# Optimization experiments

Measured on AMD Instinct MI355X. Metric: run time of the kernel, lower is better.

Reference implementation:

```python
import jax, jax.numpy as jnp
import numpy as np


def setup_inputs() -> dict:
    key = jax.random.key(0)
    k1, k2, k3, k4 = jax.random.split(key, 4)
    B, T, D = 32, 2048, 128
    queries = jax.random.normal(k1, (B, T, D), dtype=jnp.float32)
    keys = jax.random.normal(k2, (B, T, D), dtype=jnp.float32)
    values = jax.random.normal(k3, (B, T, D), dtype=jnp.float32)
    valid_lens = jax.random.randint(k4, (B,), 0, T, dtype=jnp.int32)
    return {"queries": queries, "keys": keys, "values": values, "valid_lens": valid_lens}


def reference(queries, keys, values, valid_lens):
    d = queries.shape[-1]
    scale = d / 0.5  # faithful to source: 2*d, NOT sqrt(d)
    # (B, Tq, Tk) scores
    scores = jnp.einsum('bqd,bkd->bqk', queries, keys) / scale
    T = scores.shape[-1]
    # lengths (B,) -> mask (B, 1, Tk), broadcast over query rows
    mask = jnp.arange(T) < valid_lens[:, None, None]
    neg_inf = jnp.finfo(scores.dtype).min
    logits = jnp.where(mask, scores, neg_inf)
    probs = jax.nn.softmax(logits, axis=-1)
    fully_masked = ~jnp.any(mask, axis=-1, keepdims=True)
    probs = jnp.where(fully_masked, jnp.zeros_like(probs), probs)
    # dropout p=0.0 -> identity
    return jnp.einsum('bqk,bkv->bqv', probs, values)
```

## Files before the change

kernel.cpp:

```cpp
#include <hip/hip_runtime.h>
#include <hip/hip_bf16.h>
#include <stdint.h>

#define B_ 32
#define T_ 2048
#define D_ 128
#define BQ 128
#define BK 64

typedef __attribute__((ext_vector_type(8))) __bf16 bf16x8;
typedef __attribute__((ext_vector_type(16))) float f32x16;

__device__ __forceinline__ float fast_exp2(float x) {
#if __has_builtin(__builtin_amdgcn_exp2f)
    return __builtin_amdgcn_exp2f(x);
#else
    return exp2f(x);
#endif
}

__device__ __forceinline__ f32x16 zero16() {
    f32x16 z;
    #pragma unroll
    for (int i = 0; i < 16; ++i) z[i] = 0.f;
    return z;
}

__device__ __forceinline__ uint32_t pk2(float a, float b) {
    union { __hip_bfloat16 h; unsigned short u; } ua, ub;
    ua.h = __float2bfloat16(a); ub.h = __float2bfloat16(b);
    return (uint32_t)ua.u | ((uint32_t)ub.u << 16);
}

__device__ __forceinline__ void plswap(uint32_t& a, uint32_t& b) {
    asm("v_permlane32_swap_b32 %0, %1" : "+v"(a), "+v"(b));
}

__device__ __forceinline__ void gll16(const __hip_bfloat16* g, __hip_bfloat16* lds) {
    __builtin_amdgcn_global_load_lds(
        (const __attribute__((address_space(1))) uint32_t*)g,
        (__attribute__((address_space(3))) uint32_t*)lds,
        16, 0, 0);
}

__global__ __launch_bounds__(256, 4)
void prep_k(const float* __restrict__ K, const int* __restrict__ vlens,
            __hip_bfloat16* __restrict__ Kb)
{
    const int b = blockIdx.y, k0 = blockIdx.x * 64;
    const int kmax = (vlens[b] + 63) & ~63;
    if (k0 >= kmax) return;
    const float4* src = (const float4*)(K + ((size_t)b * T_ + k0) * D_);
    uint2* dst = (uint2*)(Kb + ((size_t)b * T_ + k0) * D_);
    #pragma unroll
    for (int it = 0; it < 8; ++it) {
        int c = it * 256 + threadIdx.x;
        float4 v = src[c];
        union { __hip_bfloat16 h[4]; uint2 u; } pk;
        pk.h[0] = __float2bfloat16(v.x); pk.h[1] = __float2bfloat16(v.y);
        pk.h[2] = __float2bfloat16(v.z); pk.h[3] = __float2bfloat16(v.w);
        dst[c] = pk.u;
    }
}

__global__ __launch_bounds__(256, 2)
void prep_vt(const float* __restrict__ V, const int* __restrict__ vlens,
             __hip_bfloat16* __restrict__ VTb)
{
    __shared__ float tile[64][132];
    const int b = blockIdx.y, k0 = blockIdx.x * 64;
    const int kmax = (vlens[b] + 63) & ~63;
    if (k0 >= kmax) return;
    const float4* src = (const float4*)(V + ((size_t)b * T_ + k0) * D_);
    #pragma unroll
    for (int it = 0; it < 8; ++it) {
        int c = it * 256 + threadIdx.x;
        int row = c >> 5, c4 = c & 31;
        *(float4*)&tile[row][c4 * 4] = src[c];
    }
    __syncthreads();
    #pragma unroll
    for (int it = 0; it < 8; ++it) {
        int c = it * 256 + threadIdx.x;
        int kc = c & 15, d = c >> 4;
        union { __hip_bfloat16 h[4]; uint2 u; } pk;
        #pragma unroll
        for (int j = 0; j < 4; ++j) {
            int jj = (j + kc) & 3;
            pk.h[jj] = __float2bfloat16(tile[kc * 4 + jj][d]);
        }
        *(uint2*)(VTb + ((size_t)b * D_ + d) * T_ + k0 + kc * 4) = pk.u;
    }
}

__global__ __launch_bounds__(256, 2)
void attn_main(const float* __restrict__ Q, const int* __restrict__ vlens,
               const __hip_bfloat16* __restrict__ Kb,
               const __hip_bfloat16* __restrict__ VTb,
               float* __restrict__ out)
{
    const int tid  = threadIdx.x;
    const int wave = tid >> 6;
    const int lane = tid & 63;
    const int l32  = lane & 31;
    const int hi   = lane >> 5;

    const int b    = blockIdx.y;
    const int q0   = blockIdx.x * BQ;
    const int vlen = vlens[b];
    const int nkb  = (vlen + 63) >> 6;

    __shared__ __hip_bfloat16 sK [2][64][128];
    __shared__ __hip_bfloat16 sVT[2][128][64];

    bf16x8 qf[8];
    {
        const float* qp = Q + ((size_t)b * T_ + q0 + wave * 32 + l32) * D_ + hi * 8;
        #pragma unroll
        for (int ds = 0; ds < 8; ++ds) {
            const float4* p4 = (const float4*)(qp + ds * 16);
            float4 a = p4[0], c = p4[1];
            __hip_bfloat16 h[8] = {
                __float2bfloat16(a.x), __float2bfloat16(a.y),
                __float2bfloat16(a.z), __float2bfloat16(a.w),
                __float2bfloat16(c.x), __float2bfloat16(c.y),
                __float2bfloat16(c.z), __float2bfloat16(c.w) };
            qf[ds] = *(const bf16x8*)h;
        }
    }

    f32x16 o[4];
    #pragma unroll
    for (int dt = 0; dt < 4; ++dt) o[dt] = zero16();
    float lsum = 0.f;

    const float C = 1.4426950408889634f / 256.0f;

    const __hip_bfloat16* kb_base = Kb  + (size_t)b * T_ * D_;
    const __hip_bfloat16* vt_base = VTb + (size_t)b * D_ * T_;

    auto stage = [&](int k0s, int buf) {
        #pragma unroll
        for (int it = 0; it < 4; ++it) {
            const int blk = wave * 4 + it;
            {
                const int row = blk * 4 + (lane >> 4);
                const int s   = (lane & 15) ^ (row & 7);
                gll16(kb_base + (size_t)(k0s + row) * D_ + s * 8,
                      &sK[buf][0][0] + blk * 512);
            }
            {
                const int row = blk * 8 + (lane >> 3);
                const int s   = (lane & 7) ^ (row & 7);
                gll16(vt_base + (size_t)row * T_ + k0s + s * 8,
                      &sVT[buf][0][0] + blk * 512);
            }
        }
    };

    if (nkb > 0) stage(0, 0);
    __syncthreads();

    int cur = 0;
    for (int kb = 0; kb < nkb; ++kb) {
        const int k0 = kb * 64;

        if (kb + 1 < nkb) stage(k0 + 64, cur ^ 1);

        f32x16 s[2];
        s[0] = zero16(); s[1] = zero16();
        __builtin_amdgcn_s_setprio(1);
        #pragma unroll
        for (int ds = 0; ds < 8; ++ds) {
            const int r0 = l32, r1 = 32 + l32;
            bf16x8 kf0 = *(const bf16x8*)&sK[cur][r0][((ds * 2 + hi) ^ (r0 & 7)) * 8];
            bf16x8 kf1 = *(const bf16x8*)&sK[cur][r1][((ds * 2 + hi) ^ (r1 & 7)) * 8];
            s[0] = __builtin_amdgcn_mfma_f32_32x32x16_bf16(kf0, qf[ds], s[0], 0, 0, 0);
            s[1] = __builtin_amdgcn_mfma_f32_32x32x16_bf16(kf1, qf[ds], s[1], 0, 0, 0);
        }
        __builtin_amdgcn_s_setprio(0);

        bf16x8 pf[4];
        #pragma unroll
        for (int nt = 0; nt < 2; ++nt) {
            const int kbase_l = k0 + nt * 32 + 4 * hi;
            float p[16];
            #pragma unroll
            for (int r = 0; r < 16; ++r) {
                int krow = (r & 3) + 8 * (r >> 2);
                float e = fast_exp2(s[nt][r] * C);
                p[r] = (kbase_l + krow < vlen) ? e : 0.f;
            }
            lsum += (((p[0] + p[1]) + (p[2] + p[3])) + ((p[4] + p[5]) + (p[6] + p[7])))
                  + (((p[8] + p[9]) + (p[10] + p[11])) + ((p[12] + p[13]) + (p[14] + p[15])));
            #pragma unroll
            for (int k2 = 0; k2 < 2; ++k2) {
                const int base = k2 * 8;
                uint32_t A0 = pk2(p[base + 0], p[base + 1]);
                uint32_t B0 = pk2(p[base + 4], p[base + 5]);
                uint32_t A1 = pk2(p[base + 2], p[base + 3]);
                uint32_t B1 = pk2(p[base + 6], p[base + 7]);
                plswap(A0, B0);
                plswap(A1, B1);
                union { uint32_t u[4]; bf16x8 v; } fr;
                fr.u[0] = A0; fr.u[1] = A1; fr.u[2] = B0; fr.u[3] = B1;
                pf[nt * 2 + k2] = fr.v;
            }
        }

        __builtin_amdgcn_s_setprio(1);
        #pragma unroll
        for (int ks = 0; ks < 4; ++ks)
            #pragma unroll
            for (int dt = 0; dt < 4; ++dt) {
                const int r = dt * 32 + l32;
                bf16x8 vf = *(const bf16x8*)&sVT[cur][r][((ks * 2 + hi) ^ (r & 7)) * 8];
                o[dt] = __builtin_amdgcn_mfma_f32_32x32x16_bf16(pf[ks], vf, o[dt], 0, 0, 0);
            }
        __builtin_amdgcn_s_setprio(0);

        __syncthreads();
        cur ^= 1;
    }

    lsum += __shfl_xor(lsum, 32);
    float inv = (lsum > 0.f) ? 1.0f / lsum : 0.f;
    float invr[16];
    #pragma unroll
    for (int r = 0; r < 16; ++r)
        invr[r] = __shfl(inv, (r & 3) + 8 * (r >> 2) + 4 * hi);
    #pragma unroll
    for (int dt = 0; dt < 4; ++dt)
        #pragma unroll
        for (int r = 0; r < 16; ++r) {
            int q = (r & 3) + 8 * (r >> 2) + 4 * hi;
            out[((size_t)b * T_ + q0 + wave * 32 + q) * D_ + dt * 32 + l32] = o[dt][r] * invr[r];
        }
}

extern "C" void kernel_launch(void* const* d_in, const int* in_sizes, int n_in,
                              void* d_out, int out_size, void* d_ws, size_t ws_size,
                              hipStream_t stream) {
    const float* Q = (const float*)d_in[0];
    const float* K = (const float*)d_in[1];
    const float* V = (const float*)d_in[2];
    const int* vl  = (const int*)d_in[3];
    float* out     = (float*)d_out;

    const size_t kb_bytes = (size_t)B_ * T_ * D_ * 2;
    if (ws_size < 2 * kb_bytes) return;
    __hip_bfloat16* Kb  = (__hip_bfloat16*)d_ws;
    __hip_bfloat16* VTb = (__hip_bfloat16*)((char*)d_ws + kb_bytes);

    prep_k <<<dim3(T_ / 64, B_), 256, 0, stream>>>(K, vl, Kb);
    prep_vt<<<dim3(T_ / 64, B_), 256, 0, stream>>>(V, vl, VTb);
    attn_main<<<dim3(T_ / BQ, B_), 256, 0, stream>>>(Q, vl, Kb, VTb, out);
}
```

Measured before the change: 232.7 us.

## Use persistent atomic work queue, smaller key tiles, and fused prep kernel

Merges the K-convert and V-transpose prep kernels into one launch. The attention kernel becomes persistent with a 1024-block grid that pulls (batch, query-block) tasks from a global atomic counter, which is meant to balance the uneven work caused by varying valid lengths. The key tile drops from 64 to 32 with a new LDS swizzle, which halves shared memory so occupancy can rise to 4 blocks per SM. In exchange it adds atomic and barrier overhead per task and more loop iterations per key range. It also relies on a global counter reset by the last block, which is fragile.

```diff
diff --git a/kernel.cpp b/kernel.cpp
--- a/kernel.cpp
+++ b/kernel.cpp
@@ -6,10 +6,16 @@
 #define T_ 2048
 #define D_ 128
 #define BQ 128
-#define BK 64
+#define BK 32
+#define NQB (T_ / BQ)
+#define NTASK (B_ * NQB)
+#define GRIDP 1024
 
 typedef __attribute__((ext_vector_type(8))) __bf16 bf16x8;
 typedef __attribute__((ext_vector_type(16))) float f32x16;
+
+__device__ int g_ctr  = 0;
+__device__ int g_done = 0;
 
 __device__ __forceinline__ float fast_exp2(float x) {
 #if __has_builtin(__builtin_amdgcn_exp2f)
@@ -43,57 +49,55 @@
         16, 0, 0);
 }
 
-__global__ __launch_bounds__(256, 4)
-void prep_k(const float* __restrict__ K, const int* __restrict__ vlens,
-            __hip_bfloat16* __restrict__ Kb)
-{
-    const int b = blockIdx.y, k0 = blockIdx.x * 64;
-    const int kmax = (vlens[b] + 63) & ~63;
-    if (k0 >= kmax) return;
-    const float4* src = (const float4*)(K + ((size_t)b * T_ + k0) * D_);
-    uint2* dst = (uint2*)(Kb + ((size_t)b * T_ + k0) * D_);
-    #pragma unroll
-    for (int it = 0; it < 8; ++it) {
-        int c = it * 256 + threadIdx.x;
-        float4 v = src[c];
-        union { __hip_bfloat16 h[4]; uint2 u; } pk;
-        pk.h[0] = __float2bfloat16(v.x); pk.h[1] = __float2bfloat16(v.y);
-        pk.h[2] = __float2bfloat16(v.z); pk.h[3] = __float2bfloat16(v.w);
-        dst[c] = pk.u;
-    }
-}
-
 __global__ __launch_bounds__(256, 2)
-void prep_vt(const float* __restrict__ V, const int* __restrict__ vlens,
-             __hip_bfloat16* __restrict__ VTb)
+void prep(const float* __restrict__ K, const float* __restrict__ V,
+          const int* __restrict__ vlens,
+          __hip_bfloat16* __restrict__ Kb, __hip_bfloat16* __restrict__ VTb)
 {
     __shared__ float tile[64][132];
     const int b = blockIdx.y, k0 = blockIdx.x * 64;
     const int kmax = (vlens[b] + 63) & ~63;
     if (k0 >= kmax) return;
-    const float4* src = (const float4*)(V + ((size_t)b * T_ + k0) * D_);
-    #pragma unroll
-    for (int it = 0; it < 8; ++it) {
-        int c = it * 256 + threadIdx.x;
-        int row = c >> 5, c4 = c & 31;
-        *(float4*)&tile[row][c4 * 4] = src[c];
-    }
-    __syncthreads();
-    #pragma unroll
-    for (int it = 0; it < 8; ++it) {
-        int c = it * 256 + threadIdx.x;
-        int kc = c & 15, d = c >> 4;
-        union { __hip_bfloat16 h[4]; uint2 u; } pk;
-        #pragma unroll
-        for (int j = 0; j < 4; ++j) {
-            int jj = (j + kc) & 3;
-            pk.h[jj] = __float2bfloat16(tile[kc * 4 + jj][d]);
-        }
-        *(uint2*)(VTb + ((size_t)b * D_ + d) * T_ + k0 + kc * 4) = pk.u;
-    }
-}
-
-__global__ __launch_bounds__(256, 2)
+
+    {
+        const float4* src = (const float4*)(K + ((size_t)b * T_ + k0) * D_);
+        uint2* dst = (uint2*)(Kb + ((size_t)b * T_ + k0) * D_);
+        #pragma unroll
+        for (int it = 0; it < 8; ++it) {
+            int c = it * 256 + threadIdx.x;
+            float4 v = src[c];
+            union { __hip_bfloat16 h[4]; uint2 u; } pk;
+            pk.h[0] = __float2bfloat16(v.x); pk.h[1] = __float2bfloat16(v.y);
+            pk.h[2] = __float2bfloat16(v.z); pk.h[3] = __float2bfloat16(v.w);
+            dst[c] = pk.u;
+        }
+    }
+
+    {
+        const float4* src = (const float4*)(V + ((size_t)b * T_ + k0) * D_);
+        #pragma unroll
+        for (int it = 0; it < 8; ++it) {
+            int c = it * 256 + threadIdx.x;
+            int row = c >> 5, c4 = c & 31;
+            *(float4*)&tile[row][c4 * 4] = src[c];
+        }
+        __syncthreads();
+        #pragma unroll
+        for (int it = 0; it < 8; ++it) {
+            int c = it * 256 + threadIdx.x;
+            int kc = c & 15, d = c >> 4;
+            union { __hip_bfloat16 h[4]; uint2 u; } pk;
+            #pragma unroll
+            for (int j = 0; j < 4; ++j) {
+                int jj = (j + kc) & 3;
+                pk.h[jj] = __float2bfloat16(tile[kc * 4 + jj][d]);
+            }
+            *(uint2*)(VTb + ((size_t)b * D_ + d) * T_ + k0 + kc * 4) = pk.u;
+        }
+    }
+}
+
+__global__ __launch_bounds__(256, 4)
 void attn_main(const float* __restrict__ Q, const int* __restrict__ vlens,
                const __hip_bfloat16* __restrict__ Kb,
                const __hip_bfloat16* __restrict__ VTb,
@@ -105,137 +109,146 @@
     const int l32  = lane & 31;
     const int hi   = lane >> 5;
 
-    const int b    = blockIdx.y;
-    const int q0   = blockIdx.x * BQ;
-    const int vlen = vlens[b];
-    const int nkb  = (vlen + 63) >> 6;
-
-    __shared__ __hip_bfloat16 sK [2][64][128];
-    __shared__ __hip_bfloat16 sVT[2][128][64];
-
-    bf16x8 qf[8];
-    {
-        const float* qp = Q + ((size_t)b * T_ + q0 + wave * 32 + l32) * D_ + hi * 8;
-        #pragma unroll
-        for (int ds = 0; ds < 8; ++ds) {
-            const float4* p4 = (const float4*)(qp + ds * 16);
-            float4 a = p4[0], c = p4[1];
-            __hip_bfloat16 h[8] = {
-                __float2bfloat16(a.x), __float2bfloat16(a.y),
-                __float2bfloat16(a.z), __float2bfloat16(a.w),
-                __float2bfloat16(c.x), __float2bfloat16(c.y),
-                __float2bfloat16(c.z), __float2bfloat16(c.w) };
-            qf[ds] = *(const bf16x8*)h;
-        }
-    }
-
-    f32x16 o[4];
-    #pragma unroll
-    for (int dt = 0; dt < 4; ++dt) o[dt] = zero16();
-    float lsum = 0.f;
+    __shared__ __hip_bfloat16 sK [2][BK][128];
+    __shared__ __hip_bfloat16 sVT[2][128][BK];
+    __shared__ int s_task;
 
     const float C = 1.4426950408889634f / 256.0f;
 
-    const __hip_bfloat16* kb_base = Kb  + (size_t)b * T_ * D_;
-    const __hip_bfloat16* vt_base = VTb + (size_t)b * D_ * T_;
-
-    auto stage = [&](int k0s, int buf) {
-        #pragma unroll
-        for (int it = 0; it < 4; ++it) {
-            const int blk = wave * 4 + it;
+    for (;;) {
+        if (tid == 0) s_task = atomicAdd(&g_ctr, 1);
+        __syncthreads();
+        const int task = s_task;
+        __syncthreads();
+        if (task >= NTASK) break;
+
+        const int b    = task >> 4;
+        const int q0   = (task & (NQB - 1)) * BQ;
+        const int vlen = vlens[b];
+        const int nkb  = (vlen + BK - 1) / BK;
+
+        bf16x8 qf[8];
+        {
+            const float* qp = Q + ((size_t)b * T_ + q0 + wave * 32 + l32) * D_ + hi * 8;
+            #pragma unroll
+            for (int ds = 0; ds < 8; ++ds) {
+                const float4* p4 = (const float4*)(qp + ds * 16);
+                float4 a = p4[0], c = p4[1];
+                __hip_bfloat16 h[8] = {
+                    __float2bfloat16(a.x), __float2bfloat16(a.y),
+                    __float2bfloat16(a.z), __float2bfloat16(a.w),
+                    __float2bfloat16(c.x), __float2bfloat16(c.y),
+                    __float2bfloat16(c.z), __float2bfloat16(c.w) };
+                qf[ds] = *(const bf16x8*)h;
+            }
+        }
+
+        f32x16 o[4];
+        #pragma unroll
+        for (int dt = 0; dt < 4; ++dt) o[dt] = zero16();
+        float lsum = 0.f;
+
+        const __hip_bfloat16* kb_base = Kb  + (size_t)b * T_ * D_;
+        const __hip_bfloat16* vt_base = VTb + (size_t)b * D_ * T_;
+
+        auto stage = [&](int k0s, int buf) {
+            #pragma unroll
+            for (int it = 0; it < 2; ++it) {
+                const int blk = wave * 2 + it;
+                {
+                    const int row = blk * 4 + (lane >> 4);
+                    const int s   = (lane & 15) ^ (row & 7);
+                    gll16(kb_base + (size_t)(k0s + row) * D_ + s * 8,
+                          &sK[buf][0][0] + blk * 512);
+                }
+                {
+                    const int row = blk * 16 + (lane >> 2);
+                    const int s   = (lane & 3) ^ ((row >> 1) & 3);
+                    gll16(vt_base + (size_t)row * T_ + k0s + s * 8,
+                          &sVT[buf][0][0] + blk * 512);
+                }
+            }
+        };
+
+        if (nkb > 0) stage(0, 0);
+        __syncthreads();
+
+        int cur = 0;
+        for (int kb = 0; kb < nkb; ++kb) {
+            const int k0 = kb * BK;
+            if (kb + 1 < nkb) stage(k0 + BK, cur ^ 1);
+
+            f32x16 s0 = zero16();
+            __builtin_amdgcn_s_setprio(1);
+            #pragma unroll
+            for (int ds = 0; ds < 8; ++ds) {
+                bf16x8 kf = *(const bf16x8*)&sK[cur][l32][(((ds * 2 + hi) ^ (l32 & 7))) * 8];
+                s0 = __builtin_amdgcn_mfma_f32_32x32x16_bf16(kf, qf[ds], s0, 0, 0, 0);
+            }
+            __builtin_amdgcn_s_setprio(0);
+
+            bf16x8 pf[2];
             {
-                const int row = blk * 4 + (lane >> 4);
-                const int s   = (lane & 15) ^ (row & 7);
-                gll16(kb_base + (size_t)(k0s + row) * D_ + s * 8,
-                      &sK[buf][0][0] + blk * 512);
-            }
-            {
-                const int row = blk * 8 + (lane >> 3);
-                const int s   = (lane & 7) ^ (row & 7);
-                gll16(vt_base + (size_t)row * T_ + k0s + s * 8,
-                      &sVT[buf][0][0] + blk * 512);
-            }
-        }
-    };
-
-    if (nkb > 0) stage(0, 0);
-    __syncthreads();
-
-    int cur = 0;
-    for (int kb = 0; kb < nkb; ++kb) {
-        const int k0 = kb * 64;
-
-        if (kb + 1 < nkb) stage(k0 + 64, cur ^ 1);
-
-        f32x16 s[2];
-        s[0] = zero16(); s[1] = zero16();
-        __builtin_amdgcn_s_setprio(1);
-        #pragma unroll
-        for (int ds = 0; ds < 8; ++ds) {
-            const int r0 = l32, r1 = 32 + l32;
-            bf16x8 kf0 = *(const bf16x8*)&sK[cur][r0][((ds * 2 + hi) ^ (r0 & 7)) * 8];
-            bf16x8 kf1 = *(const bf16x8*)&sK[cur][r1][((ds * 2 + hi) ^ (r1 & 7)) * 8];
-            s[0] = __builtin_amdgcn_mfma_f32_32x32x16_bf16(kf0, qf[ds], s[0], 0, 0, 0);
-            s[1] = __builtin_amdgcn_mfma_f32_32x32x16_bf16(kf1, qf[ds], s[1], 0, 0, 0);
-        }
-        __builtin_amdgcn_s_setprio(0);
-
-        bf16x8 pf[4];
-        #pragma unroll
-        for (int nt = 0; nt < 2; ++nt) {
-            const int kbase_l = k0 + nt * 32 + 4 * hi;
-            float p[16];
+                const int kbase_l = k0 + 4 * hi;
+                float p[16];
+                #pragma unroll
+                for (int r = 0; r < 16; ++r) {
+                    int krow = (r & 3) + 8 * (r >> 2);
+                    float e = fast_exp2(s0[r] * C);
+                    p[r] = (kbase_l + krow < vlen) ? e : 0.f;
+                }
+                lsum += (((p[0] + p[1]) + (p[2] + p[3])) + ((p[4] + p[5]) + (p[6] + p[7])))
+                      + (((p[8] + p[9]) + (p[10] + p[11])) + ((p[12] + p[13]) + (p[14] + p[15])));
+                #pragma unroll
+                for (int k2 = 0; k2 < 2; ++k2) {
+                    const int base = k2 * 8;
+                    uint32_t A0 = pk2(p[base + 0], p[base + 1]);
+                    uint32_t B0 = pk2(p[base + 4], p[base + 5]);
+                    uint32_t A1 = pk2(p[base + 2], p[base + 3]);
+                    uint32_t B1 = pk2(p[base + 6], p[base + 7]);
+                    plswap(A0, B0);
+                    plswap(A1, B1);
+                    union { uint32_t u[4]; bf16x8 v; } fr;
+                    fr.u[0] = A0; fr.u[1] = A1; fr.u[2] = B0; fr.u[3] = B1;
+                    pf[k2] = fr.v;
+                }
+            }
+
+            __builtin_amdgcn_s_setprio(1);
+            #pragma unroll
+            for (int ks = 0; ks < 2; ++ks)
+                #pragma unroll
+                for (int dt = 0; dt < 4; ++dt) {
+                    const int r = dt * 32 + l32;
+                    bf16x8 vf = *(const bf16x8*)&sVT[cur][r][(((ks * 2 + hi) ^ ((r >> 1) & 3))) * 8];
+                    o[dt] = __builtin_amdgcn_mfma_f32_32x32x16_bf16(pf[ks], vf, o[dt], 0, 0, 0);
+                }
+            __builtin_amdgcn_s_setprio(0);
+
+            __syncthreads();
+            cur ^= 1;
+        }
+
+        float ls  = lsum + __shfl_xor(lsum, 32);
+        float inv = (ls > 0.f) ? 1.0f / ls : 0.f;
+        float invr[16];
+        #pragma unroll
+        for (int r = 0; r < 16; ++r)
+            invr[r] = __shfl(inv, (r & 3) + 8 * (r >> 2) + 4 * hi);
+        #pragma unroll
+        for (int dt = 0; dt < 4; ++dt)
             #pragma unroll
             for (int r = 0; r < 16; ++r) {
-                int krow = (r & 3) + 8 * (r >> 2);
-                float e = fast_exp2(s[nt][r] * C);
-                p[r] = (kbase_l + krow < vlen) ? e : 0.f;
-            }
-            lsum += (((p[0] + p[1]) + (p[2] + p[3])) + ((p[4] + p[5]) + (p[6] + p[7])))
-                  + (((p[8] + p[9]) + (p[10] + p[11])) + ((p[12] + p[13]) + (p[14] + p[15])));
-            #pragma unroll
-            for (int k2 = 0; k2 < 2; ++k2) {
-                const int base = k2 * 8;
-                uint32_t A0 = pk2(p[base + 0], p[base + 1]);
-                uint32_t B0 = pk2(p[base + 4], p[base + 5]);
-                uint32_t A1 = pk2(p[base + 2], p[base + 3]);
-                uint32_t B1 = pk2(p[base + 6], p[base + 7]);
-                plswap(A0, B0);
-                plswap(A1, B1);
-                union { uint32_t u[4]; bf16x8 v; } fr;
-                fr.u[0] = A0; fr.u[1] = A1; fr.u[2] = B0; fr.u[3] = B1;
-                pf[nt * 2 + k2] = fr.v;
-            }
-        }
-
-        __builtin_amdgcn_s_setprio(1);
-        #pragma unroll
-        for (int ks = 0; ks < 4; ++ks)
-            #pragma unroll
-            for (int dt = 0; dt < 4; ++dt) {
-                const int r = dt * 32 + l32;
-                bf16x8 vf = *(const bf16x8*)&sVT[cur][r][((ks * 2 + hi) ^ (r & 7)) * 8];
-                o[dt] = __builtin_amdgcn_mfma_f32_32x32x16_bf16(pf[ks], vf, o[dt], 0, 0, 0);
-            }
-        __builtin_amdgcn_s_setprio(0);
-
-        __syncthreads();
-        cur ^= 1;
-    }
-
-    lsum += __shfl_xor(lsum, 32);
-    float inv = (lsum > 0.f) ? 1.0f / lsum : 0.f;
-    float invr[16];
-    #pragma unroll
-    for (int r = 0; r < 16; ++r)
-        invr[r] = __shfl(inv, (r & 3) + 8 * (r >> 2) + 4 * hi);
-    #pragma unroll
-    for (int dt = 0; dt < 4; ++dt)
-        #pragma unroll
-        for (int r = 0; r < 16; ++r) {
-            int q = (r & 3) + 8 * (r >> 2) + 4 * hi;
-            out[((size_t)b * T_ + q0 + wave * 32 + q) * D_ + dt * 32 + l32] = o[dt][r] * invr[r];
-        }
+                int q = (r & 3) + 8 * (r >> 2) + 4 * hi;
+                out[((size_t)b * T_ + q0 + wave * 32 + q) * D_ + dt * 32 + l32]
+                    = o[dt][r] * invr[r];
+            }
+    }
+
+    if (tid == 0) {
+        int d = atomicAdd(&g_done, 1);
+        if (d == GRIDP - 1) { atomicExch(&g_ctr, 0); atomicExch(&g_done, 0); }
+    }
 }
 
 extern "C" void kernel_launch(void* const* d_in, const int* in_sizes, int n_in,
@@ -252,7 +265,6 @@
     __hip_bfloat16* Kb  = (__hip_bfloat16*)d_ws;
     __hip_bfloat16* VTb = (__hip_bfloat16*)((char*)d_ws + kb_bytes);
 
-    prep_k <<<dim3(T_ / 64, B_), 256, 0, stream>>>(K, vl, Kb);
-    prep_vt<<<dim3(T_ / 64, B_), 256, 0, stream>>>(V, vl, VTb);
-    attn_main<<<dim3(T_ / BQ, B_), 256, 0, stream>>>(Q, vl, Kb, VTb, out);
-}
+    prep     <<<dim3(T_ / 64, B_), 256, 0, stream>>>(K, V, vl, Kb, VTb);
+    attn_main<<<dim3(GRIDP), 256, 0, stream>>>(Q, vl, Kb, VTb, out);
+}
```

New measurement: 320.6 us. 37.7% more time.
